# Kernel tuning notes

Measured on AMD Instinct MI355X. Metric: run time of the kernel, lower is better.

## Reference

```python
import jax, jax.numpy as jnp
import numpy as np

B, T, C = 4, 2048, 1024
N_HEAD = 16
HEAD_DIM = C // N_HEAD


def setup_inputs() -> dict:
    key = jax.random.key(0)
    k1, k2, k3 = jax.random.split(key, 3)
    x = jax.random.normal(k1, (B, T, C), dtype=jnp.float32)
    # w_attn corresponds to c_attn.weight.T (shape [C, 3C]); w_proj to c_proj.weight.T ([C, C])
    w_attn = jax.random.normal(k2, (C, 3 * C), dtype=jnp.float32) * (1.0 / np.sqrt(C))
    w_proj = jax.random.normal(k3, (C, C), dtype=jnp.float32) * (1.0 / np.sqrt(C))
    return {"x": x, "w_attn": w_attn, "w_proj": w_proj}


def reference(x, w_attn, w_proj):
    Bv, Tv, Cv = x.shape
    qkv = x @ w_attn                                  # [B, T, 3C]
    q, k, v = jnp.split(qkv, 3, axis=-1)
    # [B, T, C] -> [B, H, T, Dh]
    def heads(t):
        return t.reshape(Bv, Tv, N_HEAD, HEAD_DIM).transpose(0, 2, 1, 3)
    q, k, v = heads(q), heads(k), heads(v)
    scale = 1.0 / np.sqrt(HEAD_DIM)
    att = jnp.einsum('bhqd,bhkd->bhqk', q, k) * scale   # [B, H, T, T]
    causal = jnp.tril(jnp.ones((Tv, Tv), dtype=bool))
    att = jnp.where(causal[None, None, :, :], att, -jnp.inf)
    att = jax.nn.softmax(att, axis=-1)
    y = jnp.einsum('bhqk,bhkd->bhqd', att, v)            # [B, H, T, Dh]
    y = y.transpose(0, 2, 1, 3).reshape(Bv, Tv, Cv)      # [B, T, C]
    y = y @ w_proj
    # present_kv = (k, v); return main output y plus cache, matching torch module
    return y, (k, v)
```

## Files before the change

### kernel.cpp

```cpp
#include <hip/hip_runtime.h>

#define B_  4
#define T_  2048
#define C_  1024
#define NH_ 16
#define DH_ 64

typedef __attribute__((ext_vector_type(8))) short bf16x8;
typedef __attribute__((ext_vector_type(4))) float f32x4;

__device__ __forceinline__ unsigned short f2bf(float f) {
  unsigned u = __builtin_bit_cast(unsigned, f);
  u += 0x7fffu + ((u >> 16) & 1u);
  return (unsigned short)(u >> 16);
}

__device__ __forceinline__ void gld16(const void* g, void* l) {
  __builtin_amdgcn_global_load_lds(
      (const __attribute__((address_space(1))) void*)g,
      (__attribute__((address_space(3))) void*)l, 16, 0, 0);
}

__global__ void k_cvt(const float* __restrict__ x, unsigned short* __restrict__ o, int n) {
  int i = (blockIdx.x * 256 + threadIdx.x) * 4;
  if (i < n) {
    const float4 v = *reinterpret_cast<const float4*>(x + i);
    ushort4 u;
    u.x = f2bf(v.x); u.y = f2bf(v.y); u.z = f2bf(v.z); u.w = f2bf(v.w);
    *reinterpret_cast<ushort4*>(o + i) = u;
  }
}

__global__ void k_transpose(const float* __restrict__ w, unsigned short* __restrict__ wt,
                            int K, int N) {
  __shared__ float tile[32][33];
  int tx = threadIdx.x, ty = threadIdx.y;
  int n0 = blockIdx.x * 32, k0 = blockIdx.y * 32;
  #pragma unroll
  for (int j = 0; j < 32; j += 8)
    tile[ty + j][tx] = w[(size_t)(k0 + ty + j) * N + n0 + tx];
  __syncthreads();
  #pragma unroll
  for (int j = 0; j < 32; j += 8)
    wt[(size_t)(n0 + ty + j) * K + k0 + tx] = f2bf(tile[tx][ty + j]);
}

template <int EPI>
__global__ __launch_bounds__(512, 2)
void k_gemm(const unsigned short* __restrict__ A,
            const unsigned short* __restrict__ Bt,
            int M, int N, int K,
            float* __restrict__ outF,
            unsigned short* __restrict__ qb,
            unsigned short* __restrict__ kb,
            unsigned short* __restrict__ vbT,
            float* __restrict__ kout,
            float* __restrict__ vout) {
  __shared__ __align__(16) unsigned short As[2][256 * 64];
  __shared__ __align__(16) unsigned short Bs[2][256 * 64];

  const int tid  = threadIdx.x;
  const int wave = tid >> 6;
  const int lane = tid & 63;
  const int l15  = lane & 15;
  const int quad = lane >> 4;
  const int wm   = (wave >> 2) * 128;
  const int wn   = (wave & 3) * 64;

  const int gx  = gridDim.x;
  const int lin = blockIdx.y * gx + blockIdx.x;
  const int cpx = (gx * gridDim.y) >> 3;
  const int sw  = (lin & 7) * cpx + (lin >> 3);
  const int m0  = (sw / gx) * 256;
  const int n0  = (sw % gx) * 256;

  const int cof0 = ((quad ^ (l15 & 7)) * 8);
  const int cof1 = cof0 ^ 32;

  f32x4 acc[8][4];
  #pragma unroll
  for (int i = 0; i < 8; i++)
    #pragma unroll
    for (int j = 0; j < 4; j++)
      acc[i][j] = f32x4{0.f, 0.f, 0.f, 0.f};

  auto stage_A = [&](int kt, int h) {
    unsigned short* dst = &As[kt & 1][h * 8192];
    const unsigned short* src = A + (size_t)(m0 + h * 128) * K + kt * 64;
    #pragma unroll
    for (int it = 0; it < 2; ++it) {
      int c0  = it * 512 + wave * 64;
      int c   = c0 + lane;
      int row = c >> 3;
      int scc = (c & 7) ^ (row & 7);
      gld16(src + (size_t)row * K + scc * 8, dst + c0 * 8);
    }
  };
  auto stage_B = [&](int kt, int h) {
    unsigned short* dst = &Bs[kt & 1][h * 8192];
    const unsigned short* src = Bt + (size_t)(n0 + h * 128) * K + kt * 64;
    #pragma unroll
    for (int it = 0; it < 2; ++it) {
      int c0  = it * 512 + wave * 64;
      int c   = c0 + lane;
      int row = c >> 3;
      int scc = (c & 7) ^ (row & 7);
      gld16(src + (size_t)row * K + scc * 8, dst + c0 * 8);
    }
  };

  const int NT = K >> 6;

  stage_A(0, 0); stage_A(0, 1);
  stage_B(0, 0); stage_B(0, 1);
  stage_A(1, 0); stage_A(1, 1);
  asm volatile("s_waitcnt vmcnt(4)" ::: "memory");
  __builtin_amdgcn_s_barrier();

  bf16x8 a0[4][2], a1[4][2], b0[2][2], b1[2][2];

  for (int t = 0; t < NT; ++t) {
    const unsigned short* Au = As[t & 1];
    const unsigned short* Bu = Bs[t & 1];

    #pragma unroll
    for (int mt = 0; mt < 4; mt++) {
      const unsigned short* r = Au + (wm + mt * 16 + l15) * 64;
      a0[mt][0] = *reinterpret_cast<const bf16x8*>(r + cof0);
      a0[mt][1] = *reinterpret_cast<const bf16x8*>(r + cof1);
    }
    #pragma unroll
    for (int nt = 0; nt < 2; nt++) {
      const unsigned short* r = Bu + (wn + nt * 16 + l15) * 64;
      b0[nt][0] = *reinterpret_cast<const bf16x8*>(r + cof0);
      b0[nt][1] = *reinterpret_cast<const bf16x8*>(r + cof1);
    }
    if (t + 1 < NT) stage_B(t + 1, 0);
    __builtin_amdgcn_s_barrier();
    asm volatile("s_waitcnt lgkmcnt(0)" ::: "memory");
    __builtin_amdgcn_sched_barrier(0);
    __builtin_amdgcn_s_setprio(1);
    #pragma unroll
    for (int mt = 0; mt < 4; mt++)
      #pragma unroll
      for (int nt = 0; nt < 2; nt++) {
        acc[mt][nt] = __builtin_amdgcn_mfma_f32_16x16x32_bf16(a0[mt][0], b0[nt][0], acc[mt][nt], 0, 0, 0);
        acc[mt][nt] = __builtin_amdgcn_mfma_f32_16x16x32_bf16(a0[mt][1], b0[nt][1], acc[mt][nt], 0, 0, 0);
      }
    __builtin_amdgcn_s_setprio(0);
    __builtin_amdgcn_s_barrier();

    #pragma unroll
    for (int mt = 0; mt < 4; mt++) {
      const unsigned short* r = Au + (wm + 64 + mt * 16 + l15) * 64;
      a1[mt][0] = *reinterpret_cast<const bf16x8*>(r + cof0);
      a1[mt][1] = *reinterpret_cast<const bf16x8*>(r + cof1);
    }
    if (t + 1 < NT) stage_B(t + 1, 1);
    __builtin_amdgcn_s_barrier();
    asm volatile("s_waitcnt lgkmcnt(0)" ::: "memory");
    __builtin_amdgcn_sched_barrier(0);
    __builtin_amdgcn_s_setprio(1);
    #pragma unroll
    for (int mt = 0; mt < 4; mt++)
      #pragma unroll
      for (int nt = 0; nt < 2; nt++) {
        acc[4 + mt][nt] = __builtin_amdgcn_mfma_f32_16x16x32_bf16(a1[mt][0], b0[nt][0], acc[4 + mt][nt], 0, 0, 0);
        acc[4 + mt][nt] = __builtin_amdgcn_mfma_f32_16x16x32_bf16(a1[mt][1], b0[nt][1], acc[4 + mt][nt], 0, 0, 0);
      }
    __builtin_amdgcn_s_setprio(0);
    __builtin_amdgcn_s_barrier();

    #pragma unroll
    for (int nt = 0; nt < 2; nt++) {
      const unsigned short* r = Bu + (wn + 32 + nt * 16 + l15) * 64;
      b1[nt][0] = *reinterpret_cast<const bf16x8*>(r + cof0);
      b1[nt][1] = *reinterpret_cast<const bf16x8*>(r + cof1);
    }
    if (t + 2 < NT) stage_A(t + 2, 0);
    __builtin_amdgcn_s_barrier();
    asm volatile("s_waitcnt lgkmcnt(0)" ::: "memory");
    __builtin_amdgcn_sched_barrier(0);
    __builtin_amdgcn_s_setprio(1);
    #pragma unroll
    for (int mt = 0; mt < 4; mt++)
      #pragma unroll
      for (int nt = 0; nt < 2; nt++) {
        acc[4 + mt][2 + nt] = __builtin_amdgcn_mfma_f32_16x16x32_bf16(a1[mt][0], b1[nt][0], acc[4 + mt][2 + nt], 0, 0, 0);
        acc[4 + mt][2 + nt] = __builtin_amdgcn_mfma_f32_16x16x32_bf16(a1[mt][1], b1[nt][1], acc[4 + mt][2 + nt], 0, 0, 0);
      }
    __builtin_amdgcn_s_setprio(0);
    __builtin_amdgcn_s_barrier();

    if (t + 2 < NT) stage_A(t + 2, 1);
    __builtin_amdgcn_s_barrier();
    __builtin_amdgcn_s_setprio(1);
    #pragma unroll
    for (int mt = 0; mt < 4; mt++)
      #pragma unroll
      for (int nt = 0; nt < 2; nt++) {
        acc[mt][2 + nt] = __builtin_amdgcn_mfma_f32_16x16x32_bf16(a0[mt][0], b1[nt][0], acc[mt][2 + nt], 0, 0, 0);
        acc[mt][2 + nt] = __builtin_amdgcn_mfma_f32_16x16x32_bf16(a0[mt][1], b1[nt][1], acc[mt][2 + nt], 0, 0, 0);
      }
    __builtin_amdgcn_s_setprio(0);
    if (t + 2 < NT)      { asm volatile("s_waitcnt vmcnt(4)" ::: "memory"); }
    else if (t + 1 < NT) { asm volatile("s_waitcnt vmcnt(0)" ::: "memory"); }
    __builtin_amdgcn_s_barrier();
  }

  #pragma unroll
  for (int mt = 0; mt < 8; mt++) {
    #pragma unroll
    for (int nt = 0; nt < 4; nt++) {
      #pragma unroll
      for (int r = 0; r < 4; r++) {
        float v  = acc[mt][nt][r];
        int   gm = m0 + wm + mt * 16 + quad * 4 + r;
        int   gn = n0 + wn + nt * 16 + l15;
        if constexpr (EPI == 1) {
          outF[(size_t)gm * N + gn] = v;
        } else {
          int b = gm >> 11, t2 = gm & 2047;
          int sec = gn >> 10, cn = gn & 1023;
          int h2 = cn >> 6, d = cn & 63;
          size_t idxN = (((size_t)(b * NH_ + h2)) * T_ + t2) * DH_ + d;
          size_t idxT = (((size_t)(b * NH_ + h2)) * DH_ + d) * T_ + t2;
          unsigned short bv = f2bf(v);
          if (sec == 0) { qb[idxN] = bv; }
          else if (sec == 1) { kb[idxN] = bv; kout[idxN] = v; }
          else { vbT[idxT] = bv; vout[idxN] = v; }
        }
      }
    }
  }
}

__global__ __launch_bounds__(256, 3)
void k_attn(const unsigned short* __restrict__ qb,
            const unsigned short* __restrict__ kb,
            const unsigned short* __restrict__ vbT,
            unsigned short* __restrict__ ya) {
  __shared__ __align__(16) unsigned short Ks[64 * 64];
  __shared__ __align__(16) unsigned short Vts[64 * 64];
  const int PLD = 72;
  __shared__ __align__(16) unsigned short Ps[4][16 * PLD];

  const int tid  = threadIdx.x;
  const int wave = tid >> 6;
  const int lane = tid & 63;
  const int l15  = lane & 15;
  const int quad = lane >> 4;

  const int blk  = blockIdx.x;
  const int pair = blk & 15;
  const int bh   = blk >> 4;
  const int q0p[2] = {pair * 64, (31 - pair) * 64};
  const int nkt[2] = {pair + 1, 32 - pair};
  const size_t base  = (size_t)bh * T_ * DH_;
  const size_t baseT = (size_t)bh * DH_ * T_;

  const float CS = 0.180336880f;
  const float PB = 17.3123404907f;

  bf16x8 qf[2][2];
  #pragma unroll
  for (int p = 0; p < 2; p++)
    #pragma unroll
    for (int kf = 0; kf < 2; kf++)
      qf[p][kf] = *reinterpret_cast<const bf16x8*>(
          qb + base + (size_t)(q0p[p] + wave * 16 + l15) * DH_ + kf * 32 + quad * 8);

  bf16x8 onesb;
  #pragma unroll
  for (int j = 0; j < 8; j++) onesb[j] = (short)0x3F80;

  f32x4 of[2][4], ls[2];
  #pragma unroll
  for (int p = 0; p < 2; p++) {
    ls[p] = f32x4{0.f, 0.f, 0.f, 0.f};
    #pragma unroll
    for (int nt = 0; nt < 4; nt++)
      of[p][nt] = f32x4{0.f, 0.f, 0.f, 0.f};
  }

  for (int kt = 0; kt < nkt[1]; kt++) {
    __syncthreads();
    #pragma unroll
    for (int i = 0; i < 2; i++) {
      int c0 = (wave * 2 + i) * 64;
      int c  = c0 + lane;
      gld16(kb + base + (size_t)kt * 4096 + (size_t)c * 8, &Ks[c0 * 8]);
      int row = c >> 3, col = c & 7;
      gld16(vbT + baseT + (size_t)row * T_ + kt * 64 + col * 8, &Vts[c0 * 8]);
    }
    __syncthreads();

    bf16x8 bk[4][2], vbf[4][2];
    #pragma unroll
    for (int nt = 0; nt < 4; nt++)
      #pragma unroll
      for (int kf = 0; kf < 2; kf++) {
        bk[nt][kf]  = *reinterpret_cast<const bf16x8*>(&Ks[(nt * 16 + l15) * 64 + kf * 32 + quad * 8]);
        vbf[nt][kf] = *reinterpret_cast<const bf16x8*>(&Vts[(nt * 16 + l15) * 64 + kf * 32 + quad * 8]);
      }

    #pragma unroll
    for (int p = 0; p < 2; p++) {
      if (kt >= nkt[p]) continue;

      f32x4 s[4];
      #pragma unroll
      for (int nt = 0; nt < 4; nt++) s[nt] = f32x4{0.f, 0.f, 0.f, 0.f};
      #pragma unroll
      for (int nt = 0; nt < 4; nt++)
        #pragma unroll
        for (int kf = 0; kf < 2; kf++)
          s[nt] = __builtin_amdgcn_mfma_f32_16x16x32_bf16(qf[p][kf], bk[nt][kf], s[nt], 0, 0, 0);

      if (kt == nkt[p] - 1) {
        #pragma unroll
        for (int nt = 0; nt < 4; nt++) {
          int gk = kt * 64 + nt * 16 + l15;
          #pragma unroll
          for (int r = 0; r < 4; r++) {
            int gq = q0p[p] + wave * 16 + quad * 4 + r;
            s[nt][r] = (gk <= gq) ? s[nt][r] : -3e38f;
          }
        }
      }

      #pragma unroll
      for (int nt = 0; nt < 4; nt++)
        #pragma unroll
        for (int r = 0; r < 4; r++) {
          float pv = __builtin_amdgcn_exp2f(__builtin_fmaf(s[nt][r], CS, -PB));
          Ps[wave][(quad * 4 + r) * PLD + nt * 16 + l15] = f2bf(pv);
        }

      bf16x8 pa[2];
      #pragma unroll
      for (int kf = 0; kf < 2; kf++)
        pa[kf] = *reinterpret_cast<const bf16x8*>(&Ps[wave][l15 * PLD + kf * 32 + quad * 8]);
      #pragma unroll
      for (int nt = 0; nt < 4; nt++)
        #pragma unroll
        for (int kf = 0; kf < 2; kf++)
          of[p][nt] = __builtin_amdgcn_mfma_f32_16x16x32_bf16(pa[kf], vbf[nt][kf], of[p][nt], 0, 0, 0);
      #pragma unroll
      for (int kf = 0; kf < 2; kf++)
        ls[p] = __builtin_amdgcn_mfma_f32_16x16x32_bf16(pa[kf], onesb, ls[p], 0, 0, 0);
    }
  }

  const int b = bh >> 4, h = bh & 15;
  #pragma unroll
  for (int p = 0; p < 2; p++)
    #pragma unroll
    for (int r = 0; r < 4; r++) {
      int t = q0p[p] + wave * 16 + quad * 4 + r;
      float inv = 1.f / ls[p][r];
      #pragma unroll
      for (int nt = 0; nt < 4; nt++) {
        int col = h * DH_ + nt * 16 + l15;
        ya[((size_t)(b * T_ + t)) * C_ + col] = f2bf(of[p][nt][r] * inv);
      }
    }
}

extern "C" void kernel_launch(void* const* d_in, const int* in_sizes, int n_in,
                              void* d_out, int out_size, void* d_ws, size_t ws_size,
                              hipStream_t stream) {
  const float* x      = (const float*)d_in[0];
  const float* w_attn = (const float*)d_in[1];
  const float* w_proj = (const float*)d_in[2];

  float* y    = (float*)d_out;
  float* kout = y + (size_t)B_ * T_ * C_;
  float* vout = kout + (size_t)B_ * T_ * C_;

  char* ws = (char*)d_ws;
  const size_t xe = (size_t)B_ * T_ * C_;
  unsigned short* xb  = (unsigned short*)ws;  ws += xe * 2;
  unsigned short* wab = (unsigned short*)ws;  ws += (size_t)3 * C_ * C_ * 2;
  unsigned short* wpb = (unsigned short*)ws;  ws += (size_t)C_ * C_ * 2;
  unsigned short* qbb = (unsigned short*)ws;  ws += xe * 2;
  unsigned short* kbb = (unsigned short*)ws;  ws += xe * 2;
  unsigned short* vbb = (unsigned short*)ws;  ws += xe * 2;
  unsigned short* ya  = xb;

  const int M = B_ * T_;

  k_cvt<<<(int)(xe / 4 / 256), 256, 0, stream>>>(x, xb, (int)xe);
  k_transpose<<<dim3(3 * C_ / 32, C_ / 32), dim3(32, 8), 0, stream>>>(w_attn, wab, C_, 3 * C_);
  k_transpose<<<dim3(C_ / 32, C_ / 32), dim3(32, 8), 0, stream>>>(w_proj, wpb, C_, C_);

  k_gemm<0><<<dim3(3 * C_ / 256, M / 256), 512, 0, stream>>>(
      xb, wab, M, 3 * C_, C_, nullptr, qbb, kbb, vbb, kout, vout);

  k_attn<<<dim3(B_ * NH_ * 16), 256, 0, stream>>>(qbb, kbb, vbb, ya);

  k_gemm<1><<<dim3(C_ / 256, M / 256), 512, 0, stream>>>(
      ya, wpb, M, C_, C_, y, nullptr, nullptr, nullptr, nullptr, nullptr);
}
```

Baseline: 364.6 us.

## Shrink GEMM M-tile to 128 and stage V transpose through LDS for coalesced stores

Halves the GEMM block tile in M from 256 to 128, so each block covers 128x256 with a 4-phase-to-2-phase main loop and half the accumulators. The QKV and projection grids double, which helps fill the GPU's compute units. The V-section epilogue now writes the bf16 transposed V into shared memory and stores it with 16-byte vector writes, replacing strided scalar transposed stores. The trade-offs are less data reuse per block, a launch-bounds change to one block per SM, and an extra barrier in the epilogue.

Result: faster. 327.2 us (-10.3%).

```diff
diff --git a/kernel.cpp b/kernel.cpp
--- a/kernel.cpp
+++ b/kernel.cpp
@@ -46,7 +46,7 @@
 }
 
 template <int EPI>
-__global__ __launch_bounds__(512, 2)
+__global__ __launch_bounds__(512, 1)
 void k_gemm(const unsigned short* __restrict__ A,
             const unsigned short* __restrict__ Bt,
             int M, int N, int K,
@@ -56,37 +56,36 @@
             unsigned short* __restrict__ vbT,
             float* __restrict__ kout,
             float* __restrict__ vout) {
-  __shared__ __align__(16) unsigned short As[2][256 * 64];
-  __shared__ __align__(16) unsigned short Bs[2][256 * 64];
+  __shared__ __align__(16) unsigned short SMEM[49152];
 
   const int tid  = threadIdx.x;
   const int wave = tid >> 6;
   const int lane = tid & 63;
   const int l15  = lane & 15;
   const int quad = lane >> 4;
-  const int wm   = (wave >> 2) * 128;
+  const int wm   = (wave >> 2) * 64;
   const int wn   = (wave & 3) * 64;
 
   const int gx  = gridDim.x;
   const int lin = blockIdx.y * gx + blockIdx.x;
   const int cpx = (gx * gridDim.y) >> 3;
   const int sw  = (lin & 7) * cpx + (lin >> 3);
-  const int m0  = (sw / gx) * 256;
+  const int m0  = (sw / gx) * 128;
   const int n0  = (sw % gx) * 256;
 
   const int cof0 = ((quad ^ (l15 & 7)) * 8);
   const int cof1 = cof0 ^ 32;
 
-  f32x4 acc[8][4];
-  #pragma unroll
-  for (int i = 0; i < 8; i++)
+  f32x4 acc[4][4];
+  #pragma unroll
+  for (int i = 0; i < 4; i++)
     #pragma unroll
     for (int j = 0; j < 4; j++)
       acc[i][j] = f32x4{0.f, 0.f, 0.f, 0.f};
 
-  auto stage_A = [&](int kt, int h) {
-    unsigned short* dst = &As[kt & 1][h * 8192];
-    const unsigned short* src = A + (size_t)(m0 + h * 128) * K + kt * 64;
+  auto stage_A = [&](int kt) {
+    unsigned short* dst = SMEM + (kt & 1) * 8192;
+    const unsigned short* src = A + (size_t)m0 * K + kt * 64;
     #pragma unroll
     for (int it = 0; it < 2; ++it) {
       int c0  = it * 512 + wave * 64;
@@ -97,7 +96,7 @@
     }
   };
   auto stage_B = [&](int kt, int h) {
-    unsigned short* dst = &Bs[kt & 1][h * 8192];
+    unsigned short* dst = SMEM + 16384 + (kt & 1) * 16384 + h * 8192;
     const unsigned short* src = Bt + (size_t)(n0 + h * 128) * K + kt * 64;
     #pragma unroll
     for (int it = 0; it < 2; ++it) {
@@ -111,23 +110,23 @@
 
   const int NT = K >> 6;
 
-  stage_A(0, 0); stage_A(0, 1);
+  stage_A(0);
   stage_B(0, 0); stage_B(0, 1);
-  stage_A(1, 0); stage_A(1, 1);
-  asm volatile("s_waitcnt vmcnt(4)" ::: "memory");
+  stage_A(1);
+  asm volatile("s_waitcnt vmcnt(2)" ::: "memory");
   __builtin_amdgcn_s_barrier();
 
-  bf16x8 a0[4][2], a1[4][2], b0[2][2], b1[2][2];
+  bf16x8 af[4][2], b0[2][2], b1[2][2];
 
   for (int t = 0; t < NT; ++t) {
-    const unsigned short* Au = As[t & 1];
-    const unsigned short* Bu = Bs[t & 1];
+    const unsigned short* Au = SMEM + (t & 1) * 8192;
+    const unsigned short* Bu = SMEM + 16384 + (t & 1) * 16384;
 
     #pragma unroll
     for (int mt = 0; mt < 4; mt++) {
       const unsigned short* r = Au + (wm + mt * 16 + l15) * 64;
-      a0[mt][0] = *reinterpret_cast<const bf16x8*>(r + cof0);
-      a0[mt][1] = *reinterpret_cast<const bf16x8*>(r + cof1);
+      af[mt][0] = *reinterpret_cast<const bf16x8*>(r + cof0);
+      af[mt][1] = *reinterpret_cast<const bf16x8*>(r + cof1);
     }
     #pragma unroll
     for (int nt = 0; nt < 2; nt++) {
@@ -144,19 +143,20 @@
     for (int mt = 0; mt < 4; mt++)
       #pragma unroll
       for (int nt = 0; nt < 2; nt++) {
-        acc[mt][nt] = __builtin_amdgcn_mfma_f32_16x16x32_bf16(a0[mt][0], b0[nt][0], acc[mt][nt], 0, 0, 0);
-        acc[mt][nt] = __builtin_amdgcn_mfma_f32_16x16x32_bf16(a0[mt][1], b0[nt][1], acc[mt][nt], 0, 0, 0);
+        acc[mt][nt] = __builtin_amdgcn_mfma_f32_16x16x32_bf16(af[mt][0], b0[nt][0], acc[mt][nt], 0, 0, 0);
+        acc[mt][nt] = __builtin_amdgcn_mfma_f32_16x16x32_bf16(af[mt][1], b0[nt][1], acc[mt][nt], 0, 0, 0);
       }
     __builtin_amdgcn_s_setprio(0);
     __builtin_amdgcn_s_barrier();
 
     #pragma unroll
-    for (int mt = 0; mt < 4; mt++) {
-      const unsigned short* r = Au + (wm + 64 + mt * 16 + l15) * 64;
-      a1[mt][0] = *reinterpret_cast<const bf16x8*>(r + cof0);
-      a1[mt][1] = *reinterpret_cast<const bf16x8*>(r + cof1);
+    for (int nt = 0; nt < 2; nt++) {
+      const unsigned short* r = Bu + (wn + 32 + nt * 16 + l15) * 64;
+      b1[nt][0] = *reinterpret_cast<const bf16x8*>(r + cof0);
+      b1[nt][1] = *reinterpret_cast<const bf16x8*>(r + cof1);
     }
     if (t + 1 < NT) stage_B(t + 1, 1);
+    if (t + 2 < NT) stage_A(t + 2);
     __builtin_amdgcn_s_barrier();
     asm volatile("s_waitcnt lgkmcnt(0)" ::: "memory");
     __builtin_amdgcn_sched_barrier(0);
@@ -165,72 +165,76 @@
     for (int mt = 0; mt < 4; mt++)
       #pragma unroll
       for (int nt = 0; nt < 2; nt++) {
-        acc[4 + mt][nt] = __builtin_amdgcn_mfma_f32_16x16x32_bf16(a1[mt][0], b0[nt][0], acc[4 + mt][nt], 0, 0, 0);
-        acc[4 + mt][nt] = __builtin_amdgcn_mfma_f32_16x16x32_bf16(a1[mt][1], b0[nt][1], acc[4 + mt][nt], 0, 0, 0);
+        acc[mt][2 + nt] = __builtin_amdgcn_mfma_f32_16x16x32_bf16(af[mt][0], b1[nt][0], acc[mt][2 + nt], 0, 0, 0);
+        acc[mt][2 + nt] = __builtin_amdgcn_mfma_f32_16x16x32_bf16(af[mt][1], b1[nt][1], acc[mt][2 + nt], 0, 0, 0);
       }
     __builtin_amdgcn_s_setprio(0);
-    __builtin_amdgcn_s_barrier();
-
-    #pragma unroll
-    for (int nt = 0; nt < 2; nt++) {
-      const unsigned short* r = Bu + (wn + 32 + nt * 16 + l15) * 64;
-      b1[nt][0] = *reinterpret_cast<const bf16x8*>(r + cof0);
-      b1[nt][1] = *reinterpret_cast<const bf16x8*>(r + cof1);
-    }
-    if (t + 2 < NT) stage_A(t + 2, 0);
-    __builtin_amdgcn_s_barrier();
-    asm volatile("s_waitcnt lgkmcnt(0)" ::: "memory");
-    __builtin_amdgcn_sched_barrier(0);
-    __builtin_amdgcn_s_setprio(1);
-    #pragma unroll
-    for (int mt = 0; mt < 4; mt++)
-      #pragma unroll
-      for (int nt = 0; nt < 2; nt++) {
-        acc[4 + mt][2 + nt] = __builtin_amdgcn_mfma_f32_16x16x32_bf16(a1[mt][0], b1[nt][0], acc[4 + mt][2 + nt], 0, 0, 0);
-        acc[4 + mt][2 + nt] = __builtin_amdgcn_mfma_f32_16x16x32_bf16(a1[mt][1], b1[nt][1], acc[4 + mt][2 + nt], 0, 0, 0);
-      }
-    __builtin_amdgcn_s_setprio(0);
-    __builtin_amdgcn_s_barrier();
-
-    if (t + 2 < NT) stage_A(t + 2, 1);
-    __builtin_amdgcn_s_barrier();
-    __builtin_amdgcn_s_setprio(1);
-    #pragma unroll
-    for (int mt = 0; mt < 4; mt++)
-      #pragma unroll
-      for (int nt = 0; nt < 2; nt++) {
-        acc[mt][2 + nt] = __builtin_amdgcn_mfma_f32_16x16x32_bf16(a0[mt][0], b1[nt][0], acc[mt][2 + nt], 0, 0, 0);
-        acc[mt][2 + nt] = __builtin_amdgcn_mfma_f32_16x16x32_bf16(a0[mt][1], b1[nt][1], acc[mt][2 + nt], 0, 0, 0);
-      }
-    __builtin_amdgcn_s_setprio(0);
-    if (t + 2 < NT)      { asm volatile("s_waitcnt vmcnt(4)" ::: "memory"); }
+    if (t + 2 < NT)      { asm volatile("s_waitcnt vmcnt(2)" ::: "memory"); }
     else if (t + 1 < NT) { asm volatile("s_waitcnt vmcnt(0)" ::: "memory"); }
     __builtin_amdgcn_s_barrier();
   }
 
-  #pragma unroll
-  for (int mt = 0; mt < 8; mt++) {
-    #pragma unroll
-    for (int nt = 0; nt < 4; nt++) {
-      #pragma unroll
-      for (int r = 0; r < 4; r++) {
-        float v  = acc[mt][nt][r];
-        int   gm = m0 + wm + mt * 16 + quad * 4 + r;
-        int   gn = n0 + wn + nt * 16 + l15;
-        if constexpr (EPI == 1) {
-          outF[(size_t)gm * N + gn] = v;
-        } else {
-          int b = gm >> 11, t2 = gm & 2047;
-          int sec = gn >> 10, cn = gn & 1023;
-          int h2 = cn >> 6, d = cn & 63;
-          size_t idxN = (((size_t)(b * NH_ + h2)) * T_ + t2) * DH_ + d;
-          size_t idxT = (((size_t)(b * NH_ + h2)) * DH_ + d) * T_ + t2;
-          unsigned short bv = f2bf(v);
-          if (sec == 0) { qb[idxN] = bv; }
-          else if (sec == 1) { kb[idxN] = bv; kout[idxN] = v; }
-          else { vbT[idxT] = bv; vout[idxN] = v; }
+  if constexpr (EPI == 1) {
+    #pragma unroll
+    for (int mt = 0; mt < 4; mt++)
+      #pragma unroll
+      for (int nt = 0; nt < 4; nt++)
+        #pragma unroll
+        for (int r = 0; r < 4; r++) {
+          int gm = m0 + wm + mt * 16 + quad * 4 + r;
+          int gn = n0 + wn + nt * 16 + l15;
+          outF[(size_t)gm * N + gn] = acc[mt][nt][r];
         }
-      }
+  } else {
+    const int secb = n0 >> 10;
+    if (secb == 2) {
+      const int b      = m0 >> 11;
+      const int t2base = m0 & 2047;
+      const int h2base = (n0 - 2048) >> 6;
+      #pragma unroll
+      for (int mt = 0; mt < 4; mt++)
+        #pragma unroll
+        for (int nt = 0; nt < 4; nt++) {
+          const int col  = wn + nt * 16 + l15;
+          const int cn   = (n0 - 2048) + col;
+          const int h2   = cn >> 6, d = cn & 63;
+          #pragma unroll
+          for (int r = 0; r < 4; r++) {
+            float v = acc[mt][nt][r];
+            int rowl = wm + mt * 16 + quad * 4 + r;
+            int t2   = t2base + rowl;
+            vout[(((size_t)(b * NH_ + h2)) * T_ + t2) * DH_ + d] = v;
+            SMEM[col * 136 + rowl] = f2bf(v);
+          }
+        }
+      __syncthreads();
+      #pragma unroll
+      for (int i = 0; i < 8; i++) {
+        int chunk = i * 512 + tid;
+        int col = chunk >> 4, tq = chunk & 15;
+        bf16x8 vv = *reinterpret_cast<const bf16x8*>(&SMEM[col * 136 + tq * 8]);
+        int h2 = h2base + (col >> 6), d = col & 63;
+        size_t idxT = (((size_t)(b * NH_ + h2)) * DH_ + d) * T_ + t2base + tq * 8;
+        *reinterpret_cast<bf16x8*>(vbT + idxT) = vv;
+      }
+    } else {
+      #pragma unroll
+      for (int mt = 0; mt < 4; mt++)
+        #pragma unroll
+        for (int nt = 0; nt < 4; nt++)
+          #pragma unroll
+          for (int r = 0; r < 4; r++) {
+            float v  = acc[mt][nt][r];
+            int   gm = m0 + wm + mt * 16 + quad * 4 + r;
+            int   gn = n0 + wn + nt * 16 + l15;
+            int b = gm >> 11, t2 = gm & 2047;
+            int cn = gn & 1023;
+            int h2 = cn >> 6, d = cn & 63;
+            size_t idxN = (((size_t)(b * NH_ + h2)) * T_ + t2) * DH_ + d;
+            unsigned short bv = f2bf(v);
+            if (secb == 0) { qb[idxN] = bv; }
+            else           { kb[idxN] = bv; kout[idxN] = v; }
+          }
     }
   }
 }
@@ -394,11 +398,11 @@
   k_transpose<<<dim3(3 * C_ / 32, C_ / 32), dim3(32, 8), 0, stream>>>(w_attn, wab, C_, 3 * C_);
   k_transpose<<<dim3(C_ / 32, C_ / 32), dim3(32, 8), 0, stream>>>(w_proj, wpb, C_, C_);
 
-  k_gemm<0><<<dim3(3 * C_ / 256, M / 256), 512, 0, stream>>>(
+  k_gemm<0><<<dim3(3 * C_ / 256, M / 128), 512, 0, stream>>>(
       xb, wab, M, 3 * C_, C_, nullptr, qbb, kbb, vbb, kout, vout);
 
   k_attn<<<dim3(B_ * NH_ * 16), 256, 0, stream>>>(qbb, kbb, vbb, ya);
 
-  k_gemm<1><<<dim3(C_ / 256, M / 256), 512, 0, stream>>>(
+  k_gemm<1><<<dim3(C_ / 256, M / 128), 512, 0, stream>>>(
       ya, wpb, M, C_, C_, y, nullptr, nullptr, nullptr, nullptr, nullptr);
 }
```
